# Performance work log

Hardware: AMD Instinct MI355X
Metric: run time of the kernel (lower is better)

## Reference

```python
import jax, jax.numpy as jnp
import numpy as np

N_USERS = 50000
N_BOOKS = 10000
N = N_USERS + N_BOOKS   # 60000 nodes
E = 1_200_000           # edges
D = 64                  # embedding_dim
H, C = 4, 32            # GAT heads / per-head channels (concat -> 128)
EPS = 1e-5              # BatchNorm eps
NEG_SLOPE = 0.2         # GAT leaky relu slope


def setup_inputs() -> dict:
    key = jax.random.key(0)
    ks = jax.random.split(key, 30)
    x = jax.random.normal(ks[0], (N, D), jnp.float32)
    src = jax.random.randint(ks[1], (E,), 0, N)
    dst = jax.random.randint(ks[2], (E,), 0, N)
    edge_index = jnp.stack([src, dst]).astype(jnp.int32)

    def w(k, shape, fan_in):
        return jax.random.normal(k, shape, jnp.float32) * (1.0 / np.sqrt(fan_in))

    def bn(k, n):
        k1, k2, k3, k4 = jax.random.split(k, 4)
        return (jax.random.uniform(k1, (n,), jnp.float32, 0.5, 1.5),   # gamma
                jax.random.normal(k2, (n,), jnp.float32) * 0.1,        # beta
                jax.random.normal(k3, (n,), jnp.float32) * 0.1,        # running_mean
                jax.random.uniform(k4, (n,), jnp.float32, 0.5, 1.5))   # running_var

    bn1_g, bn1_b, bn1_m, bn1_v = bn(ks[10], H * C)
    bn2_g, bn2_b, bn2_m, bn2_v = bn(ks[11], 64)
    bn3_g, bn3_b, bn3_m, bn3_v = bn(ks[12], 32)
    return {
        "x": x, "edge_index": edge_index,
        # GATConv(64 -> 32, heads=4, concat)
        "gat_w": w(ks[3], (H * C, D), D),
        "gat_att_src": w(ks[4], (H, C), C),
        "gat_att_dst": w(ks[5], (H, C), C),
        "gat_b": jnp.zeros((H * C,), jnp.float32),
        "bn1_g": bn1_g, "bn1_b": bn1_b, "bn1_m": bn1_m, "bn1_v": bn1_v,
        # SAGEConv(128 -> 64): lin_l (neighbors, with bias), lin_r (self, no bias)
        "sage_wl": w(ks[6], (64, H * C), H * C),
        "sage_bl": jnp.zeros((64,), jnp.float32),
        "sage_wr": w(ks[7], (64, H * C), H * C),
        "bn2_g": bn2_g, "bn2_b": bn2_b, "bn2_m": bn2_m, "bn2_v": bn2_v,
        # GCNConv(64 -> 32)
        "gcn_w": w(ks[8], (32, 64), 64),
        "gcn_b": jnp.zeros((32,), jnp.float32),
        "bn3_g": bn3_g, "bn3_b": bn3_b, "bn3_m": bn3_m, "bn3_v": bn3_v,
    }


def _bn_eval(h, g, b, m, v):
    return (h - m) * jax.lax.rsqrt(v + EPS) * g + b


def _segment_softmax(e, seg, n):
    # softmax of per-edge logits e [E, H] grouped by target node seg
    mx = jax.ops.segment_max(e, seg, num_segments=n)
    ex = jnp.exp(e - mx[seg])
    s = jax.ops.segment_sum(ex, seg, num_segments=n)
    return ex / (s[seg] + 1e-16)


def reference(x, edge_index, gat_w, gat_att_src, gat_att_dst, gat_b,
              bn1_g, bn1_b, bn1_m, bn1_v,
              sage_wl, sage_bl, sage_wr,
              bn2_g, bn2_b, bn2_m, bn2_v,
              gcn_w, gcn_b,
              bn3_g, bn3_b, bn3_m, bn3_v):
    n = x.shape[0]
    src, dst = edge_index[0], edge_index[1]  # messages flow src -> dst
    loop = jnp.arange(n, dtype=src.dtype)
    src_sl = jnp.concatenate([src, loop])    # with self-loops (GAT, GCN)
    dst_sl = jnp.concatenate([dst, loop])

    # ---- GATConv(64 -> 32, heads=4, concat) ----
    xw = (x @ gat_w.T).reshape(n, H, C)                      # [N, H, C]
    a_src = jnp.einsum('nhc,hc->nh', xw, gat_att_src)        # [N, H]
    a_dst = jnp.einsum('nhc,hc->nh', xw, gat_att_dst)
    logits = jax.nn.leaky_relu(a_src[src_sl] + a_dst[dst_sl], NEG_SLOPE)  # [E+N, H]
    alpha = _segment_softmax(logits, dst_sl, n)
    msg = xw[src_sl] * alpha[:, :, None]                     # [E+N, H, C]
    h = jax.ops.segment_sum(msg, dst_sl, num_segments=n).reshape(n, H * C) + gat_b
    h = _bn_eval(jax.nn.elu(h), bn1_g, bn1_b, bn1_m, bn1_v)  # dropout = eval no-op

    # ---- SAGEConv(128 -> 64), mean aggregation, no self-loops ----
    deg = jax.ops.segment_sum(jnp.ones_like(dst, jnp.float32), dst, num_segments=n)
    nbr_mean = jax.ops.segment_sum(h[src], dst, num_segments=n) / jnp.maximum(deg, 1.0)[:, None]
    h = nbr_mean @ sage_wl.T + sage_bl + h @ sage_wr.T
    h = _bn_eval(jax.nn.elu(h), bn2_g, bn2_b, bn2_m, bn2_v)

    # ---- GCNConv(64 -> 32), symmetric normalization with self-loops ----
    hw = h @ gcn_w.T                                         # [N, 32]
    deg_sl = jax.ops.segment_sum(jnp.ones_like(dst_sl, jnp.float32), dst_sl, num_segments=n)
    dinv = jnp.where(deg_sl > 0, jax.lax.rsqrt(deg_sl), 0.0)
    norm = dinv[src_sl] * dinv[dst_sl]                       # [E+N]
    h = jax.ops.segment_sum(norm[:, None] * hw[src_sl], dst_sl, num_segments=n) + gcn_b
    h = _bn_eval(jax.nn.elu(h), bn3_g, bn3_b, bn3_m, bn3_v)
    return h
```

## Files before the change

kernel.cpp:

```cpp
#include <hip/hip_runtime.h>

#define NN 60000
#define EE 1200000
#define NBK 938
#define CH  4096

typedef __attribute__((ext_vector_type(8))) short short8;
typedef __attribute__((ext_vector_type(4))) float f32x4;

__device__ __forceinline__ float leakyf(float x){ return x >= 0.f ? x : 0.2f*x; }
__device__ __forceinline__ float eluf(float x){ return x > 0.f ? x : expm1f(x); }

__device__ __forceinline__ float bflo(uint v){ union{uint i;float f;}c; c.i = v<<16; return c.f; }
__device__ __forceinline__ float bfhi(uint v){ union{uint i;float f;}c; c.i = v & 0xffff0000u; return c.f; }
__device__ __forceinline__ ushort f2bf(float f){ union{float f;uint i;}c; c.f=f;
    uint r = c.i + 0x7fffu + ((c.i>>16)&1u); return (ushort)(r>>16); }
__device__ __forceinline__ uint pack2(float a, float b){ return (uint)f2bf(a) | ((uint)f2bf(b)<<16); }
__device__ __forceinline__ short8 ld8(const uint* p){
    union{ uint4 u; short8 s; } c; c.u = *(const uint4*)p; return c.s; }

__global__ __launch_bounds__(256) void k_bcount(const int* __restrict__ dst,
                                                int* __restrict__ bhist){
    __shared__ int lh[NBK];
    int t = threadIdx.x;
    for (int j = t; j < NBK; j += 256) lh[j] = 0;
    __syncthreads();
    for (int e = blockIdx.x*256 + t; e < EE; e += gridDim.x*256)
        atomicAdd(&lh[dst[e] >> 6], 1);
    __syncthreads();
    for (int j = t; j < NBK; j += 256){
        int v = lh[j];
        if (v) atomicAdd(&bhist[j], v);
    }
}

__global__ __launch_bounds__(256) void k_prep(const int* __restrict__ bhist,
        int* __restrict__ bstart, int* __restrict__ bcur,
        const float* __restrict__ wl, const float* __restrict__ wr,
        const float* __restrict__ gcw,
        ushort* __restrict__ wcat, ushort* __restrict__ gcb){
    int blk = blockIdx.x, t = threadIdx.x;
    if (blk == 0){
        __shared__ int stmp[256];
        int vals[4], s4 = 0;
        #pragma unroll
        for (int k = 0; k < 4; k++){
            int idx = t*4 + k;
            vals[k] = (idx < NBK) ? bhist[idx] : 0;
            s4 += vals[k];
        }
        stmp[t] = s4; __syncthreads();
        for (int off = 1; off < 256; off <<= 1){
            int o = (t >= off) ? stmp[t-off] : 0;
            __syncthreads();
            stmp[t] += o;
            __syncthreads();
        }
        int ex = stmp[t] - s4;
        #pragma unroll
        for (int k = 0; k < 4; k++){
            int idx = t*4 + k;
            if (idx < NBK){ bstart[idx] = ex; bcur[idx] = ex; ex += vals[k]; }
        }
        if (t == 0) bstart[NBK] = EE;
    } else {
        int g = (blk-1)*256 + t;
        if (g < 16384){
            int o = g >> 8, k = g & 255;
            float v = (k < 128) ? wl[o*128 + k] : wr[o*128 + (k-128)];
            wcat[g] = f2bf(v);
        }
        if (g < 2048) gcb[g] = f2bf(gcw[g]);
    }
}

__global__ __launch_bounds__(256) void k_binsort(const int* __restrict__ src,
        const int* __restrict__ dst, int* __restrict__ bcur,
        int* __restrict__ pairs){
    __shared__ int hist[NBK];
    __shared__ int loff[NBK];
    __shared__ int rcur[NBK];
    __shared__ int gbase[NBK];
    __shared__ int2 buf2[CH];
    __shared__ int stmp[256];
    int t = threadIdx.x;
    for (int e0 = blockIdx.x*CH; e0 < EE; e0 += gridDim.x*CH){
        int cnt = min(CH, EE - e0);
        for (int j = t; j < NBK; j += 256){ hist[j] = 0; rcur[j] = 0; }
        __syncthreads();
        int pk[16], bb[16];
        #pragma unroll
        for (int k = 0; k < 16; k++){
            int j = t + k*256;
            bool ok = j < cnt;
            int s = 0, d = 0;
            if (ok){ s = src[e0+j]; d = dst[e0+j]; atomicAdd(&hist[d >> 6], 1); }
            pk[k] = (s << 6) | (d & 63);
            bb[k] = ok ? (d >> 6) : -1;
        }
        __syncthreads();
        int b0 = t*4, ssum = 0, hv[4];
        #pragma unroll
        for (int k2 = 0; k2 < 4; k2++){
            int idx = b0 + k2;
            hv[k2] = (idx < NBK) ? hist[idx] : 0;
            ssum += hv[k2];
        }
        stmp[t] = ssum; __syncthreads();
        for (int off = 1; off < 256; off <<= 1){
            int o = (t >= off) ? stmp[t-off] : 0;
            __syncthreads();
            stmp[t] += o;
            __syncthreads();
        }
        int excl = stmp[t] - ssum;
        #pragma unroll
        for (int k2 = 0; k2 < 4; k2++){
            int idx = b0 + k2;
            if (idx < NBK){ loff[idx] = excl; excl += hv[k2]; }
        }
        __syncthreads();
        for (int j = t; j < NBK; j += 256){
            int h = hist[j];
            if (h) gbase[j] = atomicAdd(&bcur[j], h);
        }
        __syncthreads();
        #pragma unroll
        for (int k = 0; k < 16; k++){
            int b = bb[k];
            if (b >= 0){
                int lpos = loff[b] + atomicAdd(&rcur[b], 1);
                buf2[lpos] = make_int2(pk[k], b);
            }
        }
        __syncthreads();
        for (int j = t; j < cnt; j += 256){
            int2 pr = buf2[j];
            pairs[gbase[pr.y] + (j - loff[pr.y])] = pr.x;
        }
        __syncthreads();
    }
}

__global__ __launch_bounds__(256) void k_csr_local(const int* __restrict__ bstart,
        const int* __restrict__ pairs, int* __restrict__ rp,
        int* __restrict__ col, float* __restrict__ dinv){
    __shared__ int cnt64[64];
    int b = blockIdx.x, t = threadIdx.x;
    int nb0 = b*64;
    int base = bstart[b];
    int bsz = bstart[b+1] - base;
    if (t < 64) cnt64[t] = 0;
    __syncthreads();
    for (int i = t; i < bsz; i += 256)
        atomicAdd(&cnt64[pairs[base+i] & 63], 1);
    __syncthreads();
    if (t < 64){
        int v = cnt64[t];
        int inc = v;
        #pragma unroll
        for (int d = 1; d < 64; d <<= 1){
            int o = __shfl_up(inc, d);
            if (t >= d) inc += o;
        }
        int ex = inc - v;
        int node = nb0 + t;
        if (node < NN){
            rp[node] = base + ex;
            dinv[node] = rsqrtf((float)(v + 1));
        }
        cnt64[t] = ex;
    }
    __syncthreads();
    for (int i = t; i < bsz; i += 256){
        int pv = pairs[base + i];
        int lpos = atomicAdd(&cnt64[pv & 63], 1);
        col[base + lpos] = pv >> 6;
    }
    if (b == 0 && t == 0) rp[NN] = EE;
}

#define XTILE 938
__global__ __launch_bounds__(256) void k_xw_mfma(const float* __restrict__ x,
        const float* __restrict__ w, const float* __restrict__ att_s,
        const float* __restrict__ att_d, ushort* __restrict__ xw_h,
        float* __restrict__ a_src, float* __restrict__ a_dst){
    int t = threadIdx.x;
    int wv = t >> 6, lane = t & 63;
    int l15 = lane & 15, g = lane >> 4;
    short8 bw[2][2];
    float attv_s[2], attv_d[2];
    #pragma unroll
    for (int ct = 0; ct < 2; ct++){
        int colo = wv*32 + ct*16 + l15;
        attv_s[ct] = att_s[colo];
        attv_d[ct] = att_d[colo];
        #pragma unroll
        for (int ks = 0; ks < 2; ks++){
            const float* wp = w + colo*64 + ks*32 + g*8;
            short8 b;
            #pragma unroll
            for (int j = 0; j < 8; j++) b[j] = (short)f2bf(wp[j]);
            bw[ct][ks] = b;
        }
    }
    for (int tile = blockIdx.x; tile < XTILE; tile += gridDim.x){
        int nb = tile*64;
        #pragma unroll
        for (int rt = 0; rt < 4; rt++){
            int na = nb + rt*16 + l15;
            const float* xp = x + (size_t)min(na, NN-1)*64;
            short8 a[2];
            #pragma unroll
            for (int ks = 0; ks < 2; ks++){
                float xv[8];
                *(float4*)&xv[0] = *(const float4*)(xp + ks*32 + g*8);
                *(float4*)&xv[4] = *(const float4*)(xp + ks*32 + g*8 + 4);
                short8 av;
                #pragma unroll
                for (int j = 0; j < 8; j++) av[j] = (short)f2bf(xv[j]);
                a[ks] = av;
            }
            f32x4 acc0 = {0.f,0.f,0.f,0.f}, acc1 = {0.f,0.f,0.f,0.f};
            acc0 = __builtin_amdgcn_mfma_f32_16x16x32_bf16(a[0], bw[0][0], acc0, 0, 0, 0);
            acc0 = __builtin_amdgcn_mfma_f32_16x16x32_bf16(a[1], bw[0][1], acc0, 0, 0, 0);
            acc1 = __builtin_amdgcn_mfma_f32_16x16x32_bf16(a[0], bw[1][0], acc1, 0, 0, 0);
            acc1 = __builtin_amdgcn_mfma_f32_16x16x32_bf16(a[1], bw[1][1], acc1, 0, 0, 0);
            #pragma unroll
            for (int r = 0; r < 4; r++){
                int node = nb + rt*16 + g*4 + r;
                if (node < NN){
                    xw_h[(size_t)node*128 + wv*32 + l15]      = f2bf(acc0[r]);
                    xw_h[(size_t)node*128 + wv*32 + 16 + l15] = f2bf(acc1[r]);
                }
            }
            float ps[4], pd[4];
            #pragma unroll
            for (int r = 0; r < 4; r++){
                ps[r] = acc0[r]*attv_s[0] + acc1[r]*attv_s[1];
                pd[r] = acc0[r]*attv_d[0] + acc1[r]*attv_d[1];
            }
            #pragma unroll
            for (int d = 1; d < 16; d <<= 1){
                #pragma unroll
                for (int r = 0; r < 4; r++){
                    ps[r] += __shfl_xor(ps[r], d);
                    pd[r] += __shfl_xor(pd[r], d);
                }
            }
            if (l15 == 0){
                #pragma unroll
                for (int r = 0; r < 4; r++){
                    int node = nb + rt*16 + g*4 + r;
                    if (node < NN){
                        a_src[node*4 + wv] = ps[r];
                        a_dst[node*4 + wv] = pd[r];
                    }
                }
            }
        }
    }
}

__global__ __launch_bounds__(256) void k_gat(const int* __restrict__ rp,
        const int* __restrict__ col, const float* __restrict__ a_src,
        const float* __restrict__ a_dst, const uint* __restrict__ xw_u,
        const float* __restrict__ gb,
        const float* __restrict__ g1, const float* __restrict__ b1,
        const float* __restrict__ m1, const float* __restrict__ v1,
        ushort* __restrict__ h1_h){
    int gw = (blockIdx.x*256 + threadIdx.x) >> 6;
    int nwaves = (gridDim.x*256) >> 6;
    int lane = threadIdx.x & 63;
    int hh = lane >> 4;
    int o0 = 2*lane, o1 = o0 + 1;
    float gb0 = gb[o0], gb1 = gb[o1];
    float sc0 = g1[o0]*rsqrtf(v1[o0]+1e-5f), sh0 = b1[o0] - m1[o0]*sc0;
    float sc1 = g1[o1]*rsqrtf(v1[o1]+1e-5f), sh1 = b1[o1] - m1[o1]*sc1;

    for (int n = gw; n < NN; n += nwaves){
        int r0 = rp[n], deg = rp[n+1] - r0;
        float adh = a_dst[n*4 + hh];
        float wself = __expf(leakyf(a_src[n*4 + hh] + adh));
        uint v = xw_u[(size_t)n*64 + lane];
        float s  = wself;
        float ax = bflo(v)*wself, ay = bfhi(v)*wself;
        #pragma unroll 4
        for (int i = 0; i < deg; i++){
            int sidx = col[r0+i];
            float wgt = __expf(leakyf(a_src[sidx*4 + hh] + adh));
            uint vv = xw_u[(size_t)sidx*64 + lane];
            s  += wgt;
            ax += wgt*bflo(vv); ay += wgt*bfhi(vv);
        }
        float Sinv = 1.f/(s + 1e-16f);
        ax = ax*Sinv + gb0; ay = ay*Sinv + gb1;
        ax = eluf(ax)*sc0 + sh0;
        ay = eluf(ay)*sc1 + sh1;
        *(uint*)(h1_h + (size_t)n*128 + o0) = pack2(ax, ay);
    }
}

__global__ __launch_bounds__(256) void k_mean(const int* __restrict__ rp,
        const int* __restrict__ col, const uint* __restrict__ h1_u,
        uint* __restrict__ mean_u){
    int gw = (blockIdx.x*256 + threadIdx.x) >> 6;
    int nwaves = (gridDim.x*256) >> 6;
    int lane = threadIdx.x & 63;
    for (int n = gw; n < NN; n += nwaves){
        int r0 = rp[n], deg = rp[n+1] - r0;
        float ax = 0.f, ay = 0.f;
        #pragma unroll 4
        for (int i = 0; i < deg; i++){
            uint v = h1_u[(size_t)col[r0+i]*64 + lane];
            ax += bflo(v); ay += bfhi(v);
        }
        float inv = deg > 0 ? 1.f/(float)deg : 0.f;
        mean_u[(size_t)n*64 + lane] = pack2(ax*inv, ay*inv);
    }
}

#define STILE 938
__global__ __launch_bounds__(256) void k_sage_mfma(
        const uint* __restrict__ mean_u, const uint* __restrict__ h1_u,
        const uint* __restrict__ wcat_u, const float* __restrict__ bl,
        const uint* __restrict__ gcb_u,
        const float* __restrict__ g2, const float* __restrict__ b2,
        const float* __restrict__ m2, const float* __restrict__ v2,
        ushort* __restrict__ hw_h)
{
    __shared__ ushort h2_s[64][72];
    int t = threadIdx.x;
    int w = t >> 6, lane = t & 63;
    int l15 = lane & 15, g = lane >> 4;
    int olane = w*16 + l15;

    short8 bw[8];
    #pragma unroll
    for (int ks = 0; ks < 8; ks++)
        bw[ks] = ld8(wcat_u + (size_t)olane*128 + ks*16 + g*4);
    short8 bg[2][2];
    #pragma unroll
    for (int ct = 0; ct < 2; ct++)
        #pragma unroll
        for (int ks = 0; ks < 2; ks++)
            bg[ct][ks] = ld8(gcb_u + (size_t)(ct*16 + l15)*32 + ks*16 + g*4);

    float blv = bl[olane];
    float scv = g2[olane]*rsqrtf(v2[olane]+1e-5f);
    float shv = b2[olane] - m2[olane]*scv;

    for (int tile = blockIdx.x; tile < STILE; tile += gridDim.x){
        int nb = tile*64;
        __syncthreads();
        #pragma unroll
        for (int rt = 0; rt < 4; rt++){
            f32x4 acc = {0.f, 0.f, 0.f, 0.f};
            size_t node = (size_t)(nb + rt*16 + l15);
            const uint* am = mean_u + node*64 + g*4;
            const uint* as = h1_u  + node*64 + g*4;
            #pragma unroll
            for (int ks = 0; ks < 4; ks++)
                acc = __builtin_amdgcn_mfma_f32_16x16x32_bf16(ld8(am + ks*16), bw[ks], acc, 0, 0, 0);
            #pragma unroll
            for (int ks = 0; ks < 4; ks++)
                acc = __builtin_amdgcn_mfma_f32_16x16x32_bf16(ld8(as + ks*16), bw[4+ks], acc, 0, 0, 0);
            #pragma unroll
            for (int r = 0; r < 4; r++){
                int row = rt*16 + g*4 + r;
                h2_s[row][olane] = f2bf(eluf(acc[r] + blv)*scv + shv);
            }
        }
        __syncthreads();
        short8 a2[2];
        #pragma unroll
        for (int ks = 0; ks < 2; ks++)
            a2[ks] = *(const short8*)&h2_s[w*16 + l15][ks*32 + g*8];
        #pragma unroll
        for (int ct = 0; ct < 2; ct++){
            f32x4 acc2 = {0.f, 0.f, 0.f, 0.f};
            #pragma unroll
            for (int ks = 0; ks < 2; ks++)
                acc2 = __builtin_amdgcn_mfma_f32_16x16x32_bf16(a2[ks], bg[ct][ks], acc2, 0, 0, 0);
            #pragma unroll
            for (int r = 0; r < 4; r++){
                int row = nb + w*16 + g*4 + r;
                if (row < NN) hw_h[(size_t)row*32 + ct*16 + l15] = f2bf(acc2[r]);
            }
        }
    }
}

__global__ __launch_bounds__(256) void k_gcn(const int* __restrict__ rp,
        const int* __restrict__ col, const uint* __restrict__ hw_u,
        const float* __restrict__ dinv, const float* __restrict__ gb,
        const float* __restrict__ g3, const float* __restrict__ b3,
        const float* __restrict__ m3, const float* __restrict__ v3,
        float* __restrict__ out){
    int t = threadIdx.x;
    int n = blockIdx.x*4 + (t >> 6);
    int lane = t & 63, u = lane & 15, part = lane >> 4;
    int r0 = rp[n], deg = rp[n+1] - r0;
    float dn = dinv[n];
    float ax = 0.f, ay = 0.f;
    for (int i = part; i < deg; i += 4){
        int s = col[r0+i];
        float dv = dinv[s];
        uint hv = hw_u[(size_t)s*16 + u];
        ax += dv*bflo(hv); ay += dv*bfhi(hv);
    }
    ax += __shfl_xor(ax, 16); ay += __shfl_xor(ay, 16);
    ax += __shfl_xor(ax, 32); ay += __shfl_xor(ay, 32);
    if (part == 0){
        uint sv = hw_u[(size_t)n*16 + u];
        float tx = ax*dn + dn*dn*bflo(sv);
        float ty = ay*dn + dn*dn*bfhi(sv);
        int o0 = 2*u, o1 = o0 + 1;
        tx += gb[o0]; ty += gb[o1];
        tx = eluf(tx); ty = eluf(ty);
        tx = (tx - m3[o0]) * rsqrtf(v3[o0] + 1e-5f) * g3[o0] + b3[o0];
        ty = (ty - m3[o1]) * rsqrtf(v3[o1] + 1e-5f) * g3[o1] + b3[o1];
        *(float2*)(out + (size_t)n*32 + o0) = make_float2(tx, ty);
    }
}

extern "C" void kernel_launch(void* const* d_in, const int* in_sizes, int n_in,
                              void* d_out, int out_size, void* d_ws, size_t ws_size,
                              hipStream_t stream)
{
    const float* x     = (const float*)d_in[0];
    const int*   ei    = (const int*)d_in[1];
    const float* gat_w = (const float*)d_in[2];
    const float* att_s = (const float*)d_in[3];
    const float* att_d = (const float*)d_in[4];
    const float* gat_b = (const float*)d_in[5];
    const float* bn1g = (const float*)d_in[6],  *bn1b = (const float*)d_in[7];
    const float* bn1m = (const float*)d_in[8],  *bn1v = (const float*)d_in[9];
    const float* sage_wl = (const float*)d_in[10];
    const float* sage_bl = (const float*)d_in[11];
    const float* sage_wr = (const float*)d_in[12];
    const float* bn2g = (const float*)d_in[13], *bn2b = (const float*)d_in[14];
    const float* bn2m = (const float*)d_in[15], *bn2v = (const float*)d_in[16];
    const float* gcn_w = (const float*)d_in[17];
    const float* gcn_b = (const float*)d_in[18];
    const float* bn3g = (const float*)d_in[19], *bn3b = (const float*)d_in[20];
    const float* bn3m = (const float*)d_in[21], *bn3v = (const float*)d_in[22];

    const int* src  = ei;
    const int* dstp = ei + EE;

    char* W = (char*)d_ws;
    ushort* xw_h   = (ushort*)W;
    ushort* h1_h   = xw_h + (size_t)NN*128;
    ushort* mean_h = h1_h + (size_t)NN*128;
    ushort* hw_h   = mean_h + (size_t)NN*128;
    float* a_s  = (float*)(hw_h + (size_t)NN*32 + 8192);
    float* a_d  = a_s + (size_t)NN*4;
    float* dinv = a_d + (size_t)NN*4;
    int* row_ptr = (int*)(dinv + NN);
    int* col     = row_ptr + (NN+1);
    ushort* wcat_h = (ushort*)(col + EE);
    ushort* gcb_h  = wcat_h + 16384;
    int* bhist  = (int*)(gcb_h + 2048);
    int* bstart = bhist + NBK;
    int* bcur   = bstart + NBK + 1;
    char* p2 = (char*)(bcur + NBK);
    p2 = (char*)(((uintptr_t)p2 + 15) & ~(uintptr_t)15);
    int* pairs = (int*)p2;

    const uint* xw_u   = (const uint*)xw_h;
    const uint* h1_u   = (const uint*)h1_h;
    uint* mean_u = (uint*)mean_h;
    uint* hw_u   = (uint*)hw_h;
    const uint* wcat_u = (const uint*)wcat_h;
    const uint* gcb_u  = (const uint*)gcb_h;
    float* out = (float*)d_out;

    hipMemsetAsync(bhist, 0, NBK*sizeof(int), stream);
    k_bcount<<<256, 256, 0, stream>>>(dstp, bhist);
    k_prep<<<65, 256, 0, stream>>>(bhist, bstart, bcur, sage_wl, sage_wr, gcn_w,
                                   wcat_h, gcb_h);
    k_binsort<<<256, 256, 0, stream>>>(src, dstp, bcur, pairs);
    k_csr_local<<<NBK, 256, 0, stream>>>(bstart, pairs, row_ptr, col, dinv);

    k_xw_mfma<<<XTILE, 256, 0, stream>>>(x, gat_w, att_s, att_d, xw_h, a_s, a_d);
    k_gat<<<2048, 256, 0, stream>>>(row_ptr, col, a_s, a_d, xw_u, gat_b,
                                    bn1g, bn1b, bn1m, bn1v, h1_h);
    k_mean<<<2048, 256, 0, stream>>>(row_ptr, col, h1_u, mean_u);
    k_sage_mfma<<<STILE, 256, 0, stream>>>(mean_u, h1_u, wcat_u, sage_bl, gcb_u,
                                           bn2g, bn2b, bn2m, bn2v, hw_h);
    k_gcn<<<NN/4, 256, 0, stream>>>(row_ptr, col, hw_u, dinv, gcn_b,
                                    bn3g, bn3b, bn3m, bn3v, out);
}
```

Measured before the change: 254.5 us.

## Fuse SAGE neighbor-mean gather into SAGE/GCN MFMA kernel via shared memory

The separate neighbor-mean kernel and the SAGE MFMA kernel become one kernel. Each block gathers mean rows for 32 nodes into shared memory, then runs the SAGE and GCN-weight MFMAs on them directly. This removes the global round-trip of the mean buffer (write plus reread) and one kernel launch. In exchange the grid becomes one block per 32 nodes, with per-block weight loads and a barrier between the irregular gather and the matmul phase, which can reduce latency hiding.

```diff
diff --git a/kernel.cpp b/kernel.cpp
--- a/kernel.cpp
+++ b/kernel.cpp
@@ -301,13 +301,27 @@
     }
 }
 
-__global__ __launch_bounds__(256) void k_mean(const int* __restrict__ rp,
-        const int* __restrict__ col, const uint* __restrict__ h1_u,
-        uint* __restrict__ mean_u){
-    int gw = (blockIdx.x*256 + threadIdx.x) >> 6;
-    int nwaves = (gridDim.x*256) >> 6;
-    int lane = threadIdx.x & 63;
-    for (int n = gw; n < NN; n += nwaves){
+__global__ __launch_bounds__(256) void k_sage_fused(
+        const int* __restrict__ rp, const int* __restrict__ col,
+        const uint* __restrict__ h1_u,
+        const uint* __restrict__ wcat_u, const float* __restrict__ bl,
+        const uint* __restrict__ gcb_u,
+        const float* __restrict__ g2, const float* __restrict__ b2,
+        const float* __restrict__ m2, const float* __restrict__ v2,
+        ushort* __restrict__ hw_h)
+{
+    __shared__ uint mean_s[32][65];
+    __shared__ ushort h2_s[32][72];
+    int t = threadIdx.x;
+    int w = t >> 6, lane = t & 63;
+    int l15 = lane & 15, g = lane >> 4;
+    int olane = w*16 + l15;
+    int nb = blockIdx.x*32;
+
+    #pragma unroll 2
+    for (int ni = 0; ni < 8; ni++){
+        int loc = w*8 + ni;
+        int n = nb + loc;
         int r0 = rp[n], deg = rp[n+1] - r0;
         float ax = 0.f, ay = 0.f;
         #pragma unroll 4
@@ -316,78 +330,54 @@
             ax += bflo(v); ay += bfhi(v);
         }
         float inv = deg > 0 ? 1.f/(float)deg : 0.f;
-        mean_u[(size_t)n*64 + lane] = pack2(ax*inv, ay*inv);
-    }
-}
-
-#define STILE 938
-__global__ __launch_bounds__(256) void k_sage_mfma(
-        const uint* __restrict__ mean_u, const uint* __restrict__ h1_u,
-        const uint* __restrict__ wcat_u, const float* __restrict__ bl,
-        const uint* __restrict__ gcb_u,
-        const float* __restrict__ g2, const float* __restrict__ b2,
-        const float* __restrict__ m2, const float* __restrict__ v2,
-        ushort* __restrict__ hw_h)
-{
-    __shared__ ushort h2_s[64][72];
-    int t = threadIdx.x;
-    int w = t >> 6, lane = t & 63;
-    int l15 = lane & 15, g = lane >> 4;
-    int olane = w*16 + l15;
+        mean_s[loc][lane] = pack2(ax*inv, ay*inv);
+    }
 
     short8 bw[8];
     #pragma unroll
     for (int ks = 0; ks < 8; ks++)
         bw[ks] = ld8(wcat_u + (size_t)olane*128 + ks*16 + g*4);
-    short8 bg[2][2];
-    #pragma unroll
-    for (int ct = 0; ct < 2; ct++)
-        #pragma unroll
-        for (int ks = 0; ks < 2; ks++)
-            bg[ct][ks] = ld8(gcb_u + (size_t)(ct*16 + l15)*32 + ks*16 + g*4);
-
+    int ct2 = w & 1, rt2 = w >> 1;
+    short8 bg2[2];
+    #pragma unroll
+    for (int ks = 0; ks < 2; ks++)
+        bg2[ks] = ld8(gcb_u + (size_t)(ct2*16 + l15)*32 + ks*16 + g*4);
     float blv = bl[olane];
     float scv = g2[olane]*rsqrtf(v2[olane]+1e-5f);
     float shv = b2[olane] - m2[olane]*scv;
-
-    for (int tile = blockIdx.x; tile < STILE; tile += gridDim.x){
-        int nb = tile*64;
-        __syncthreads();
-        #pragma unroll
-        for (int rt = 0; rt < 4; rt++){
-            f32x4 acc = {0.f, 0.f, 0.f, 0.f};
-            size_t node = (size_t)(nb + rt*16 + l15);
-            const uint* am = mean_u + node*64 + g*4;
-            const uint* as = h1_u  + node*64 + g*4;
-            #pragma unroll
-            for (int ks = 0; ks < 4; ks++)
-                acc = __builtin_amdgcn_mfma_f32_16x16x32_bf16(ld8(am + ks*16), bw[ks], acc, 0, 0, 0);
-            #pragma unroll
-            for (int ks = 0; ks < 4; ks++)
-                acc = __builtin_amdgcn_mfma_f32_16x16x32_bf16(ld8(as + ks*16), bw[4+ks], acc, 0, 0, 0);
-            #pragma unroll
-            for (int r = 0; r < 4; r++){
-                int row = rt*16 + g*4 + r;
-                h2_s[row][olane] = f2bf(eluf(acc[r] + blv)*scv + shv);
-            }
-        }
-        __syncthreads();
-        short8 a2[2];
-        #pragma unroll
-        for (int ks = 0; ks < 2; ks++)
-            a2[ks] = *(const short8*)&h2_s[w*16 + l15][ks*32 + g*8];
-        #pragma unroll
-        for (int ct = 0; ct < 2; ct++){
-            f32x4 acc2 = {0.f, 0.f, 0.f, 0.f};
-            #pragma unroll
-            for (int ks = 0; ks < 2; ks++)
-                acc2 = __builtin_amdgcn_mfma_f32_16x16x32_bf16(a2[ks], bg[ct][ks], acc2, 0, 0, 0);
-            #pragma unroll
-            for (int r = 0; r < 4; r++){
-                int row = nb + w*16 + g*4 + r;
-                if (row < NN) hw_h[(size_t)row*32 + ct*16 + l15] = f2bf(acc2[r]);
-            }
-        }
+    __syncthreads();
+
+    #pragma unroll
+    for (int rt = 0; rt < 2; rt++){
+        f32x4 acc = {0.f, 0.f, 0.f, 0.f};
+        const uint* lm = &mean_s[rt*16 + l15][g*4];
+        const uint* as = h1_u + (size_t)(nb + rt*16 + l15)*64 + g*4;
+        #pragma unroll
+        for (int ks = 0; ks < 4; ks++)
+            acc = __builtin_amdgcn_mfma_f32_16x16x32_bf16(ld8(lm + ks*16), bw[ks], acc, 0, 0, 0);
+        #pragma unroll
+        for (int ks = 0; ks < 4; ks++)
+            acc = __builtin_amdgcn_mfma_f32_16x16x32_bf16(ld8(as + ks*16), bw[4+ks], acc, 0, 0, 0);
+        #pragma unroll
+        for (int r = 0; r < 4; r++){
+            int row = rt*16 + g*4 + r;
+            h2_s[row][olane] = f2bf(eluf(acc[r] + blv)*scv + shv);
+        }
+    }
+    __syncthreads();
+
+    short8 a2[2];
+    #pragma unroll
+    for (int ks = 0; ks < 2; ks++)
+        a2[ks] = *(const short8*)&h2_s[rt2*16 + l15][ks*32 + g*8];
+    f32x4 acc2 = {0.f, 0.f, 0.f, 0.f};
+    #pragma unroll
+    for (int ks = 0; ks < 2; ks++)
+        acc2 = __builtin_amdgcn_mfma_f32_16x16x32_bf16(a2[ks], bg2[ks], acc2, 0, 0, 0);
+    #pragma unroll
+    for (int r = 0; r < 4; r++){
+        int row = nb + rt2*16 + g*4 + r;
+        hw_h[(size_t)row*32 + ct2*16 + l15] = f2bf(acc2[r]);
     }
 }
 
@@ -452,8 +442,7 @@
     char* W = (char*)d_ws;
     ushort* xw_h   = (ushort*)W;
     ushort* h1_h   = xw_h + (size_t)NN*128;
-    ushort* mean_h = h1_h + (size_t)NN*128;
-    ushort* hw_h   = mean_h + (size_t)NN*128;
+    ushort* hw_h   = h1_h + (size_t)NN*128;
     float* a_s  = (float*)(hw_h + (size_t)NN*32 + 8192);
     float* a_d  = a_s + (size_t)NN*4;
     float* dinv = a_d + (size_t)NN*4;
@@ -470,7 +459,6 @@
 
     const uint* xw_u   = (const uint*)xw_h;
     const uint* h1_u   = (const uint*)h1_h;
-    uint* mean_u = (uint*)mean_h;
     uint* hw_u   = (uint*)hw_h;
     const uint* wcat_u = (const uint*)wcat_h;
     const uint* gcb_u  = (const uint*)gcb_h;
@@ -486,9 +474,8 @@
     k_xw_mfma<<<XTILE, 256, 0, stream>>>(x, gat_w, att_s, att_d, xw_h, a_s, a_d);
     k_gat<<<2048, 256, 0, stream>>>(row_ptr, col, a_s, a_d, xw_u, gat_b,
                                     bn1g, bn1b, bn1m, bn1v, h1_h);
-    k_mean<<<2048, 256, 0, stream>>>(row_ptr, col, h1_u, mean_u);
-    k_sage_mfma<<<STILE, 256, 0, stream>>>(mean_u, h1_u, wcat_u, sage_bl, gcb_u,
-                                           bn2g, bn2b, bn2m, bn2v, hw_h);
+    k_sage_fused<<<NN/32, 256, 0, stream>>>(row_ptr, col, h1_u, wcat_u, sage_bl,
+                                            gcb_u, bn2g, bn2b, bn2m, bn2v, hw_h);
     k_gcn<<<NN/4, 256, 0, stream>>>(row_ptr, col, hw_u, dinv, gcn_b,
                                     bn3g, bn3b, bn3m, bn3v, out);
 }
```

Result: slower. 273.3 us (+7.4%).
